# Performance work log

Hardware: AMD Instinct MI355X
Metric: run time of the kernel (lower is better)

## Reference

```python
import jax, jax.numpy as jnp
import numpy as np

OUT_FEATURES = 8192
IN_FEATURES = 4096  # d
CODEBOOK_SIZE = 16  # 2**bits, bits=4
BATCH = 32


def setup_inputs() -> dict:
    key = jax.random.key(0)
    k_x, k_idx, k_cb, k_r, k_b = jax.random.split(key, 5)
    x = jax.random.normal(k_x, (BATCH, IN_FEATURES), dtype=jnp.float32)
    indices = jax.random.randint(k_idx, (OUT_FEATURES, IN_FEATURES), 0, CODEBOOK_SIZE, dtype=jnp.int32)
    codebook = jax.random.normal(k_cb, (CODEBOOK_SIZE,), dtype=jnp.float32)
    # rotation matrix from the quantizer (orthogonal in the real impl; random here,
    # scaled for numerical stability)
    rotation_matrix = jax.random.normal(k_r, (IN_FEATURES, IN_FEATURES), dtype=jnp.float32) / np.sqrt(IN_FEATURES).astype(np.float32)
    bias = jax.random.normal(k_b, (OUT_FEATURES,), dtype=jnp.float32)
    return {"x": x, "indices": indices, "codebook": codebook,
            "rotation_matrix": rotation_matrix, "bias": bias}


def reference(x, indices, codebook, rotation_matrix, bias):
    # Dequantize: gather per-element codewords, then rotate back to weight space.
    # quantize was idx = Q(R @ w_row)  =>  w_row \approx R^T @ codebook[idx]
    codes = codebook[indices]                      # [O, D] gather
    weight = jnp.matmul(codes, rotation_matrix)    # [O, D]  (== (R^T @ c) per row)
    # F.linear(x, W, b) = x @ W^T + b
    return jnp.matmul(x, weight.T) + bias          # [B, O]
```

## Files before the change

kernel.cpp:

```cpp
#include <hip/hip_runtime.h>
#include <hip/hip_bf16.h>


#define IN_F 4096
#define OUT_F 8192
#define BATCH 32
#define TS 264

typedef short bf16x8s __attribute__((ext_vector_type(8)));
typedef float f32x4 __attribute__((ext_vector_type(4)));

__device__ __forceinline__ unsigned short f2bf(float f) {
    union { float f; unsigned int u; } v; v.f = f;
    unsigned int u = v.u;
    return (unsigned short)((u + 0x7fffu + ((u >> 16) & 1u)) >> 16);
}

__global__ void __launch_bounds__(256, 3) k1_xRT(const float* __restrict__ x,
                                                 const float* __restrict__ R,
                                                 const float* __restrict__ bias,
                                                 float* __restrict__ out,
                                                 float* __restrict__ y_ws) {
    __shared__ unsigned short Bl[64 * TS];
    __shared__ unsigned short Al[32 * TS];

    const int tid  = threadIdx.x;
    const int jt   = blockIdx.x & 63;
    const int kq   = blockIdx.x >> 6;
    const int j0   = jt * 64;
    const int k0   = kq * 256;
    const int wave = tid >> 6, lane = tid & 63;
    const int n = lane & 15, quad = lane >> 4;

    {
        int id = blockIdx.x * 256 + tid;
        out[id] = bias[id & (OUT_F - 1)];
    }

    #pragma unroll
    for (int jj = 0; jj < 16; ++jj) {
        int f = tid + jj * 256;
        int row = f >> 6, c4 = f & 63;
        const float4 v = *(const float4*)(R + (size_t)(j0 + row) * IN_F + k0 + c4 * 4);
        ushort4 pv;
        pv.x = f2bf(v.x); pv.y = f2bf(v.y); pv.z = f2bf(v.z); pv.w = f2bf(v.w);
        *(ushort4*)&Bl[row * TS + c4 * 4] = pv;
    }
    #pragma unroll
    for (int ii = 0; ii < 8; ++ii) {
        int f = tid + ii * 256;
        int row = f >> 6, c4 = f & 63;
        const float4 v = *(const float4*)(x + (size_t)row * IN_F + k0 + c4 * 4);
        ushort4 pv;
        pv.x = f2bf(v.x); pv.y = f2bf(v.y); pv.z = f2bf(v.z); pv.w = f2bf(v.w);
        *(ushort4*)&Al[row * TS + c4 * 4] = pv;
    }
    __syncthreads();

    f32x4 acc0 = {0.f, 0.f, 0.f, 0.f};
    f32x4 acc1 = {0.f, 0.f, 0.f, 0.f};
    #pragma unroll
    for (int ks = 0; ks < 8; ++ks) {
        bf16x8s bfr = *(const bf16x8s*)&Bl[(wave * 16 + n) * TS + ks * 32 + quad * 8];
        bf16x8s a0  = *(const bf16x8s*)&Al[n * TS + ks * 32 + quad * 8];
        bf16x8s a1  = *(const bf16x8s*)&Al[(16 + n) * TS + ks * 32 + quad * 8];
        acc0 = __builtin_amdgcn_mfma_f32_16x16x32_bf16(a0, bfr, acc0, 0, 0, 0);
        acc1 = __builtin_amdgcn_mfma_f32_16x16x32_bf16(a1, bfr, acc1, 0, 0, 0);
    }

    const int jcol = j0 + wave * 16 + n;
    #pragma unroll
    for (int r = 0; r < 4; ++r) {
        int br = quad * 4 + r;
        atomicAdd(&y_ws[(size_t)br * IN_F + jcol], acc0[r]);
        atomicAdd(&y_ws[(size_t)(br + 16) * IN_F + jcol], acc1[r]);
    }
}

__global__ void __launch_bounds__(256, 3) k2_out(const int* __restrict__ idx,
                                                 const float* __restrict__ cb,
                                                 const float* __restrict__ yws,
                                                 float* __restrict__ out) {
    __shared__ unsigned short Bl[64 * TS];
    __shared__ unsigned short Al[32 * TS];
    __shared__ unsigned int cbp[256];

    const int tid = threadIdx.x;

    {
        unsigned int lo = f2bf(cb[tid & 15]);
        unsigned int hi = f2bf(cb[tid >> 4]);
        cbp[tid] = lo | (hi << 16);
    }

    const int ot = blockIdx.x & 127;
    const int kq = blockIdx.x >> 7;
    const int o0 = ot * 64;
    const int k0 = kq * 256;
    const int wave = tid >> 6, lane = tid & 63;
    const int n = lane & 15, quad = lane >> 4;

    __syncthreads();

    #pragma unroll
    for (int jj = 0; jj < 16; ++jj) {
        int f = tid + jj * 256;
        int row = f >> 6, c4 = f & 63;
        const int4 iv = *(const int4*)(idx + (size_t)(o0 + row) * IN_F + k0 + c4 * 4);
        unsigned int key0 = (unsigned int)iv.x | ((unsigned int)iv.y << 4);
        unsigned int key1 = (unsigned int)iv.z | ((unsigned int)iv.w << 4);
        uint2 pv;
        pv.x = cbp[key0];
        pv.y = cbp[key1];
        *(uint2*)&Bl[row * TS + c4 * 4] = pv;
    }
    #pragma unroll
    for (int ii = 0; ii < 8; ++ii) {
        int f = tid + ii * 256;
        int row = f >> 6, c4 = f & 63;
        const float4 v = *(const float4*)(yws + (size_t)row * IN_F + k0 + c4 * 4);
        ushort4 pv;
        pv.x = f2bf(v.x); pv.y = f2bf(v.y); pv.z = f2bf(v.z); pv.w = f2bf(v.w);
        *(ushort4*)&Al[row * TS + c4 * 4] = pv;
    }
    __syncthreads();

    f32x4 acc0 = {0.f, 0.f, 0.f, 0.f};
    f32x4 acc1 = {0.f, 0.f, 0.f, 0.f};
    #pragma unroll
    for (int ks = 0; ks < 8; ++ks) {
        bf16x8s bfr = *(const bf16x8s*)&Bl[(wave * 16 + n) * TS + ks * 32 + quad * 8];
        bf16x8s a0  = *(const bf16x8s*)&Al[n * TS + ks * 32 + quad * 8];
        bf16x8s a1  = *(const bf16x8s*)&Al[(16 + n) * TS + ks * 32 + quad * 8];
        acc0 = __builtin_amdgcn_mfma_f32_16x16x32_bf16(a0, bfr, acc0, 0, 0, 0);
        acc1 = __builtin_amdgcn_mfma_f32_16x16x32_bf16(a1, bfr, acc1, 0, 0, 0);
    }

    const int ocol = o0 + wave * 16 + n;
    #pragma unroll
    for (int r = 0; r < 4; ++r) {
        int br = quad * 4 + r;
        atomicAdd(&out[(size_t)br * OUT_F + ocol], acc0[r]);
        atomicAdd(&out[(size_t)(br + 16) * OUT_F + ocol], acc1[r]);
    }
}

extern "C" void kernel_launch(void* const* d_in, const int* in_sizes, int n_in,
                              void* d_out, int out_size, void* d_ws, size_t ws_size,
                              hipStream_t stream) {
    (void)in_sizes; (void)n_in; (void)out_size; (void)ws_size;
    const float* x       = (const float*)d_in[0];
    const int*   indices = (const int*)d_in[1];
    const float* cb      = (const float*)d_in[2];
    const float* R       = (const float*)d_in[3];
    const float* bias    = (const float*)d_in[4];
    float* out  = (float*)d_out;
    float* y_ws = (float*)d_ws;

    hipMemsetAsync(y_ws, 0, (size_t)BATCH * IN_F * sizeof(float), stream);
    k1_xRT<<<dim3(1024), dim3(256), 0, stream>>>(x, R, bias, out, y_ws);
    k2_out<<<dim3(2048), dim3(256), 0, stream>>>(indices, cb, y_ws, out);
}
```

Measured before the change: 251.0 us.

## Fuse both GEMM stages into one persistent-ticket kernel with flag-based dependencies

```diff
diff --git a/kernel.cpp b/kernel.cpp
--- a/kernel.cpp
+++ b/kernel.cpp
@@ -9,6 +9,7 @@
 
 typedef short bf16x8s __attribute__((ext_vector_type(8)));
 typedef float f32x4 __attribute__((ext_vector_type(4)));
+typedef int   i32x4 __attribute__((ext_vector_type(4)));
 
 __device__ __forceinline__ unsigned short f2bf(float f) {
     union { float f; unsigned int u; } v; v.f = f;
@@ -16,132 +17,135 @@
     return (unsigned short)((u + 0x7fffu + ((u >> 16) & 1u)) >> 16);
 }
 
-__global__ void __launch_bounds__(256, 3) k1_xRT(const float* __restrict__ x,
-                                                 const float* __restrict__ R,
-                                                 const float* __restrict__ bias,
-                                                 float* __restrict__ out,
-                                                 float* __restrict__ y_ws) {
-    __shared__ unsigned short Bl[64 * TS];
-    __shared__ unsigned short Al[32 * TS];
+__global__ void __launch_bounds__(256, 3) fused(const float* __restrict__ x,
+                                                const int* __restrict__ idx,
+                                                const float* __restrict__ cb,
+                                                const float* __restrict__ R,
+                                                const float* __restrict__ bias,
+                                                float* __restrict__ out,
+                                                float* __restrict__ y_ws,
+                                                int* __restrict__ flags,
+                                                int* __restrict__ ticket) {
+    __shared__ unsigned short smem[96 * TS];
+    __shared__ unsigned int cbp[256];
+    __shared__ int t_sh;
 
-    const int tid  = threadIdx.x;
-    const int jt   = blockIdx.x & 63;
-    const int kq   = blockIdx.x >> 6;
-    const int j0   = jt * 64;
-    const int k0   = kq * 256;
+    const int tid = threadIdx.x;
+    if (tid == 0)
+        t_sh = __hip_atomic_fetch_add(ticket, 1, __ATOMIC_RELAXED, __HIP_MEMORY_SCOPE_AGENT);
+    cbp[tid] = (unsigned int)f2bf(cb[tid & 15]) | ((unsigned int)f2bf(cb[tid >> 4]) << 16);
+    __syncthreads();
+    const int t = t_sh;
+
+    const int jt  = t >> 4;
+    const int kq1 = t & 15;
+    const int ot  = t & 127;
+    const int kq2 = t >> 7;
+    const int j0 = jt * 32, k1_0 = kq1 * 256;
+    const int o0 = ot * 64, k2_0 = kq2 * 256;
     const int wave = tid >> 6, lane = tid & 63;
     const int n = lane & 15, quad = lane >> 4;
 
-    {
-        int id = blockIdx.x * 256 + tid;
-        out[id] = bias[id & (OUT_F - 1)];
-    }
-
+    i32x4 iv[16];
     #pragma unroll
     for (int jj = 0; jj < 16; ++jj) {
         int f = tid + jj * 256;
         int row = f >> 6, c4 = f & 63;
-        const float4 v = *(const float4*)(R + (size_t)(j0 + row) * IN_F + k0 + c4 * 4);
-        ushort4 pv;
-        pv.x = f2bf(v.x); pv.y = f2bf(v.y); pv.z = f2bf(v.z); pv.w = f2bf(v.w);
-        *(ushort4*)&Bl[row * TS + c4 * 4] = pv;
+        iv[jj] = __builtin_nontemporal_load(
+            (const i32x4*)(idx + (size_t)(o0 + row) * IN_F + k2_0 + c4 * 4));
     }
+
+    f32x4 rv[8], xv[8];
     #pragma unroll
     for (int ii = 0; ii < 8; ++ii) {
         int f = tid + ii * 256;
         int row = f >> 6, c4 = f & 63;
-        const float4 v = *(const float4*)(x + (size_t)row * IN_F + k0 + c4 * 4);
+        rv[ii] = __builtin_nontemporal_load(
+            (const f32x4*)(R + (size_t)(j0 + row) * IN_F + k1_0 + c4 * 4));
+        xv[ii] = *(const f32x4*)(x + (size_t)row * IN_F + k1_0 + c4 * 4);
+    }
+    unsigned short* Rl = smem;
+    unsigned short* Xl = smem + 32 * TS;
+    #pragma unroll
+    for (int ii = 0; ii < 8; ++ii) {
+        int f = tid + ii * 256;
+        int row = f >> 6, c4 = f & 63;
+        ushort4 pr, px;
+        pr.x = f2bf(rv[ii].x); pr.y = f2bf(rv[ii].y); pr.z = f2bf(rv[ii].z); pr.w = f2bf(rv[ii].w);
+        px.x = f2bf(xv[ii].x); px.y = f2bf(xv[ii].y); px.z = f2bf(xv[ii].z); px.w = f2bf(xv[ii].w);
+        *(ushort4*)&Rl[row * TS + c4 * 4] = pr;
+        *(ushort4*)&Xl[row * TS + c4 * 4] = px;
+    }
+    __syncthreads();
+
+    {
+        const int nh = wave & 1, mh = wave >> 1;
+        f32x4 acc = {0.f, 0.f, 0.f, 0.f};
+        #pragma unroll
+        for (int ks = 0; ks < 8; ++ks) {
+            bf16x8s bfr = *(const bf16x8s*)&Rl[(nh * 16 + n) * TS + ks * 32 + quad * 8];
+            bf16x8s a   = *(const bf16x8s*)&Xl[(mh * 16 + n) * TS + ks * 32 + quad * 8];
+            acc = __builtin_amdgcn_mfma_f32_16x16x32_bf16(a, bfr, acc, 0, 0, 0);
+        }
+        const int jcol = j0 + nh * 16 + n;
+        #pragma unroll
+        for (int r = 0; r < 4; ++r)
+            atomicAdd(&y_ws[(size_t)(mh * 16 + quad * 4 + r) * IN_F + jcol], acc[r]);
+    }
+    __threadfence();
+    __syncthreads();
+    if (tid == 0)
+        __hip_atomic_fetch_add(&flags[jt >> 3], 1, __ATOMIC_RELEASE, __HIP_MEMORY_SCOPE_AGENT);
+
+    unsigned short* Bl = smem;
+    unsigned short* Al = smem + 64 * TS;
+    #pragma unroll
+    for (int jj = 0; jj < 16; ++jj) {
+        int f = tid + jj * 256;
+        int row = f >> 6, c4 = f & 63;
+        unsigned int key0 = (unsigned int)iv[jj].x | ((unsigned int)iv[jj].y << 4);
+        unsigned int key1 = (unsigned int)iv[jj].z | ((unsigned int)iv[jj].w << 4);
+        uint2 pv;
+        pv.x = cbp[key0];
+        pv.y = cbp[key1];
+        *(uint2*)&Bl[row * TS + c4 * 4] = pv;
+    }
+
+    if (tid == 0) {
+        while (__hip_atomic_load(&flags[kq2], __ATOMIC_RELAXED, __HIP_MEMORY_SCOPE_AGENT) < 128)
+            __builtin_amdgcn_s_sleep(2);
+    }
+    __syncthreads();
+    __threadfence();
+
+    #pragma unroll
+    for (int ii = 0; ii < 8; ++ii) {
+        int f = tid + ii * 256;
+        int row = f >> 6, c4 = f & 63;
+        const f32x4 v = *(const f32x4*)(y_ws + (size_t)row * IN_F + k2_0 + c4 * 4);
         ushort4 pv;
         pv.x = f2bf(v.x); pv.y = f2bf(v.y); pv.z = f2bf(v.z); pv.w = f2bf(v.w);
         *(ushort4*)&Al[row * TS + c4 * 4] = pv;
     }
     __syncthreads();
 
-    f32x4 acc0 = {0.f, 0.f, 0.f, 0.f};
-    f32x4 acc1 = {0.f, 0.f, 0.f, 0.f};
+    f32x4 c0 = {0.f, 0.f, 0.f, 0.f};
+    f32x4 c1 = {0.f, 0.f, 0.f, 0.f};
     #pragma unroll
     for (int ks = 0; ks < 8; ++ks) {
         bf16x8s bfr = *(const bf16x8s*)&Bl[(wave * 16 + n) * TS + ks * 32 + quad * 8];
         bf16x8s a0  = *(const bf16x8s*)&Al[n * TS + ks * 32 + quad * 8];
         bf16x8s a1  = *(const bf16x8s*)&Al[(16 + n) * TS + ks * 32 + quad * 8];
-        acc0 = __builtin_amdgcn_mfma_f32_16x16x32_bf16(a0, bfr, acc0, 0, 0, 0);
-        acc1 = __builtin_amdgcn_mfma_f32_16x16x32_bf16(a1, bfr, acc1, 0, 0, 0);
+        c0 = __builtin_amdgcn_mfma_f32_16x16x32_bf16(a0, bfr, c0, 0, 0, 0);
+        c1 = __builtin_amdgcn_mfma_f32_16x16x32_bf16(a1, bfr, c1, 0, 0, 0);
     }
-
-    const int jcol = j0 + wave * 16 + n;
+    const int ocol = o0 + wave * 16 + n;
+    const float bv = (kq2 == 0) ? bias[ocol] : 0.f;
     #pragma unroll
     for (int r = 0; r < 4; ++r) {
         int br = quad * 4 + r;
-        atomicAdd(&y_ws[(size_t)br * IN_F + jcol], acc0[r]);
-        atomicAdd(&y_ws[(size_t)(br + 16) * IN_F + jcol], acc1[r]);
-    }
-}
-
-__global__ void __launch_bounds__(256, 3) k2_out(const int* __restrict__ idx,
-                                                 const float* __restrict__ cb,
-                                                 const float* __restrict__ yws,
-                                                 float* __restrict__ out) {
-    __shared__ unsigned short Bl[64 * TS];
-    __shared__ unsigned short Al[32 * TS];
-    __shared__ unsigned int cbp[256];
-
-    const int tid = threadIdx.x;
-
-    {
-        unsigned int lo = f2bf(cb[tid & 15]);
-        unsigned int hi = f2bf(cb[tid >> 4]);
-        cbp[tid] = lo | (hi << 16);
-    }
-
-    const int ot = blockIdx.x & 127;
-    const int kq = blockIdx.x >> 7;
-    const int o0 = ot * 64;
-    const int k0 = kq * 256;
-    const int wave = tid >> 6, lane = tid & 63;
-    const int n = lane & 15, quad = lane >> 4;
-
-    __syncthreads();
-
-    #pragma unroll
-    for (int jj = 0; jj < 16; ++jj) {
-        int f = tid + jj * 256;
-        int row = f >> 6, c4 = f & 63;
-        const int4 iv = *(const int4*)(idx + (size_t)(o0 + row) * IN_F + k0 + c4 * 4);
-        unsigned int key0 = (unsigned int)iv.x | ((unsigned int)iv.y << 4);
-        unsigned int key1 = (unsigned int)iv.z | ((unsigned int)iv.w << 4);
-        uint2 pv;
-        pv.x = cbp[key0];
-        pv.y = cbp[key1];
-        *(uint2*)&Bl[row * TS + c4 * 4] = pv;
-    }
-    #pragma unroll
-    for (int ii = 0; ii < 8; ++ii) {
-        int f = tid + ii * 256;
-        int row = f >> 6, c4 = f & 63;
-        const float4 v = *(const float4*)(yws + (size_t)row * IN_F + k0 + c4 * 4);
-        ushort4 pv;
-        pv.x = f2bf(v.x); pv.y = f2bf(v.y); pv.z = f2bf(v.z); pv.w = f2bf(v.w);
-        *(ushort4*)&Al[row * TS + c4 * 4] = pv;
-    }
-    __syncthreads();
-
-    f32x4 acc0 = {0.f, 0.f, 0.f, 0.f};
-    f32x4 acc1 = {0.f, 0.f, 0.f, 0.f};
-    #pragma unroll
-    for (int ks = 0; ks < 8; ++ks) {
-        bf16x8s bfr = *(const bf16x8s*)&Bl[(wave * 16 + n) * TS + ks * 32 + quad * 8];
-        bf16x8s a0  = *(const bf16x8s*)&Al[n * TS + ks * 32 + quad * 8];
-        bf16x8s a1  = *(const bf16x8s*)&Al[(16 + n) * TS + ks * 32 + quad * 8];
-        acc0 = __builtin_amdgcn_mfma_f32_16x16x32_bf16(a0, bfr, acc0, 0, 0, 0);
-        acc1 = __builtin_amdgcn_mfma_f32_16x16x32_bf16(a1, bfr, acc1, 0, 0, 0);
-    }
-
-    const int ocol = o0 + wave * 16 + n;
-    #pragma unroll
-    for (int r = 0; r < 4; ++r) {
-        int br = quad * 4 + r;
-        atomicAdd(&out[(size_t)br * OUT_F + ocol], acc0[r]);
-        atomicAdd(&out[(size_t)(br + 16) * OUT_F + ocol], acc1[r]);
+        atomicAdd(&out[(size_t)br * OUT_F + ocol], c0[r] + bv);
+        atomicAdd(&out[(size_t)(br + 16) * OUT_F + ocol], c1[r] + bv);
     }
 }
 
@@ -156,8 +160,11 @@
     const float* bias    = (const float*)d_in[4];
     float* out  = (float*)d_out;
     float* y_ws = (float*)d_ws;
+    int*  flags  = (int*)((char*)d_ws + 512 * 1024);
+    int*  ticket = (int*)((char*)d_ws + 512 * 1024 + 64);
 
-    hipMemsetAsync(y_ws, 0, (size_t)BATCH * IN_F * sizeof(float), stream);
-    k1_xRT<<<dim3(1024), dim3(256), 0, stream>>>(x, R, bias, out, y_ws);
-    k2_out<<<dim3(2048), dim3(256), 0, stream>>>(indices, cb, y_ws, out);
+    hipMemsetAsync(d_ws, 0, 512 * 1024 + 128, stream);
+    hipMemsetAsync(out, 0, (size_t)BATCH * OUT_F * sizeof(float), stream);
+    fused<<<dim3(2048), dim3(256), 0, stream>>>(x, indices, cb, R, bias,
+                                                out, y_ws, flags, ticket);
 }
```

After: 864.7 us. 3.45x slower.
